# Kernel optimization log

Hardware: AMD Instinct MI355X
Metric: run time of the kernel (lower is better)

## Reference

```python
import jax, jax.numpy as jnp
import numpy as np

# Jamba mamba mixer dims
H = 4096      # hidden_size
D = 8192      # intermediate_size = mamba_expand * hidden_size
N = 16        # ssm_state_size (mamba_d_state)
K = 4         # conv_kernel_size (mamba_d_conv)
R = 256       # time_step_rank (mamba_dt_rank)
BATCH = 1
L = 2048
EPS = 1e-6


def setup_inputs() -> dict:
    key = jax.random.key(0)
    ks = jax.random.split(key, 10)
    s = 0.02
    return {
        "hidden_states": jax.random.normal(ks[0], (BATCH, L, H), jnp.float32),
        "W_in": jax.random.normal(ks[1], (2 * D, H), jnp.float32) * s,
        "conv_w": jax.random.normal(ks[2], (D, K), jnp.float32) * s,
        "conv_b": jax.random.normal(ks[3], (D,), jnp.float32) * s,
        "Wx": jax.random.normal(ks[4], (R + 2 * N, D), jnp.float32) * s,
        "dt_ln_w": jnp.ones((R,), jnp.float32),
        "b_ln_w": jnp.ones((N,), jnp.float32),
        "c_ln_w": jnp.ones((N,), jnp.float32),
        "Wdt": jax.random.normal(ks[5], (D, R), jnp.float32) * s,
        "dt_bias": jax.random.normal(ks[6], (D,), jnp.float32) * s,
        "A": -jnp.exp(jax.random.normal(ks[7], (D, N), jnp.float32) * 0.5),  # A = -exp(A_log)
        "D_param": jnp.ones((D,), jnp.float32),
        "W_out": jax.random.normal(ks[8], (H, D), jnp.float32) * s,
    }


def _rmsnorm(x, w):
    return x * jax.lax.rsqrt(jnp.mean(x * x, axis=-1, keepdims=True) + EPS) * w


def reference(hidden_states, W_in, conv_w, conv_b, Wx, dt_ln_w, b_ln_w, c_ln_w,
              Wdt, dt_bias, A, D_param, W_out):
    # in_proj -> [B, L, 2D]; split into ssm branch and gate
    proj = hidden_states @ W_in.T
    u, gate = jnp.split(proj, 2, axis=-1)

    # causal depthwise conv1d over sequence dim, then SiLU (causal_conv1d_fn)
    x = jnp.transpose(u, (0, 2, 1))  # [B, D, L]
    x = jax.lax.conv_general_dilated(
        x, conv_w[:, None, :], window_strides=(1,), padding=[(K - 1, 0)],
        dimension_numbers=("NCH", "OIH", "NCH"), feature_group_count=D)
    u = jax.nn.silu(jnp.transpose(x, (0, 2, 1)) + conv_b)  # [B, L, D]

    # x_proj -> dt / B / C with RMSNorms
    ssm_p = u @ Wx.T  # [B, L, R + 2N]
    dt, Bm, Cm = jnp.split(ssm_p, [R, R + N], axis=-1)
    dt = _rmsnorm(dt, dt_ln_w)
    Bm = _rmsnorm(Bm, b_ln_w)
    Cm = _rmsnorm(Cm, c_ln_w)

    # dt_proj (skip_bias_add: bias folded into softplus, delta_softplus=True)
    delta = jax.nn.softplus(dt @ Wdt.T + dt_bias)  # [B, L, D]

    # selective scan: state [B, D, N], recurrence over L
    def step(state, xs):
        d_t, B_t, C_t, u_t = xs  # [B,D], [B,N], [B,N], [B,D]
        dA = jnp.exp(d_t[..., None] * A)                       # [B, D, N]
        state = dA * state + (d_t * u_t)[..., None] * B_t[:, None, :]
        y_t = jnp.einsum("bdn,bn->bd", state, C_t)
        return state, y_t

    init = jnp.zeros((hidden_states.shape[0], D, N), hidden_states.dtype)
    xs = (jnp.swapaxes(delta, 0, 1), jnp.swapaxes(Bm, 0, 1),
          jnp.swapaxes(Cm, 0, 1), jnp.swapaxes(u, 0, 1))
    _, ys = jax.lax.scan(step, init, xs)  # ys: [L, B, D]

    y = jnp.swapaxes(ys, 0, 1) + u * D_param   # skip connection u * D
    y = y * jax.nn.silu(gate)                  # gated output
    return y @ W_out.T                         # out_proj -> [B, L, H]
```

## Files before the change

### kernel.cpp

```cpp
#include <hip/hip_runtime.h>
#include <stdint.h>


#define LSEQ 2048
#define HDIM 4096
#define DDIM 8192
#define NST  16
#define NPAD 384
#define NC   16
#define CLEN 128

typedef __bf16 bf16x8 __attribute__((ext_vector_type(8)));
typedef float  f32x4  __attribute__((ext_vector_type(4)));

__device__ __forceinline__ ushort f2b(float f) {
  uint32_t x = __float_as_uint(f);
  x += 0x7FFFu + ((x >> 16) & 1u);
  return (ushort)(x >> 16);
}
__device__ __forceinline__ float b2f(ushort u) {
  return __uint_as_float(((uint32_t)u) << 16);
}

__device__ __forceinline__ void gload_lds16(const ushort* g, ushort* l) {
  __builtin_amdgcn_global_load_lds(
      (const __attribute__((address_space(1))) void*)g,
      (__attribute__((address_space(3))) void*)l, 16, 0, 0);
}

__global__ __launch_bounds__(256) void cvt_kernel(const float* __restrict__ s,
                                                  ushort* __restrict__ d,
                                                  size_t n8) {
  size_t i = (size_t)blockIdx.x * 256 + threadIdx.x;
  if (i >= n8) return;
  const float4* sp = (const float4*)s;
  float4 a = sp[2 * i], b = sp[2 * i + 1];
  union { ushort us[8]; uint4 v; } u;
  u.us[0] = f2b(a.x); u.us[1] = f2b(a.y); u.us[2] = f2b(a.z); u.us[3] = f2b(a.w);
  u.us[4] = f2b(b.x); u.us[5] = f2b(b.y); u.us[6] = f2b(b.z); u.us[7] = f2b(b.w);
  ((uint4*)d)[i] = u.v;
}

template <int MODE, int OUT>
__global__ __launch_bounds__(512, 2) void gemm8p(
    const ushort* __restrict__ A, const ushort* __restrict__ Bw,
    void* __restrict__ Cv, int M, int N, int ldk, int Kc) {
  __shared__ __align__(16) ushort As[2][256 * 64];
  __shared__ __align__(16) ushort Bs[2][256 * 64];
  const int tid  = threadIdx.x;
  const int lane = tid & 63;
  const int w    = tid >> 6;
  const int wr   = w >> 2;
  const int wc   = w & 3;

  const int glob = (blockIdx.z * gridDim.y + blockIdx.y) * gridDim.x + blockIdx.x;
  const int k8 = glob & 7, j = glob >> 3;
  int mt, nt, zz;
  if (MODE == 0) {
    mt = j & 7;
    nt = k8 * (gridDim.x >> 3) + (j >> 3);
    zz = 0;
  } else {
    mt = j & 7;
    nt = (k8 >> 1) * 4 + (j >> 3);
    zz = k8 & 1;
  }
  const int m0 = mt * 256, n0 = nt * 256;
  const int kbeg = zz * Kc;
  const int NT = Kc >> 6;

  const int srck = (lane & 7) ^ ((lane >> 3) & 7);
  const int astripe = w >> 2, awl = w & 3;
  const int arow_st = astripe * 128 + awl * 8 + (lane >> 3);
  const ushort* Abase = A + (size_t)(m0 + arow_st) * ldk + kbeg + srck * 8;
  const int aldsb = (astripe * 128 + awl * 8) * 64;
  const int brow_st = w * 8 + (lane >> 3);
  const ushort* Bbase = Bw + (size_t)(n0 + brow_st) * ldk + kbeg + srck * 8;
  const int bldsb = (w * 8) * 64;

  const int lrow = lane & 15;
  const int kch  = lane >> 4;
  const int axor = lrow & 7;

  auto stA = [&](int buf, int kt, int q) {
    gload_lds16(Abase + (size_t)q * 32 * ldk + kt * 64,
                &As[buf][aldsb + q * 32 * 64]);
  };
  auto stB = [&](int buf, int kt, int half, int jj) {
    gload_lds16(Bbase + (size_t)(half * 128 + jj * 64) * ldk + kt * 64,
                &Bs[buf][bldsb + (half * 128 + jj * 64) * 64]);
  };
  auto rdA = [&](int buf, int mi, int sl) -> bf16x8 {
    int arow = wr * 128 + mi * 16 + lrow;
    int s4 = sl * 4 + kch;
    return *(const bf16x8*)&As[buf][arow * 64 + ((s4 ^ axor) << 3)];
  };
  auto rdB = [&](int buf, int ni, int sl) -> bf16x8 {
    int brow = wc * 64 + ni * 16 + lrow;
    int s4 = sl * 4 + kch;
    return *(const bf16x8*)&Bs[buf][brow * 64 + ((s4 ^ axor) << 3)];
  };

  f32x4 acc[8][4] = {};
  bf16x8 afr[2][2][2];
  bf16x8 bfr[2][4][2];

#define RDAQ(BUF, Q, AP)                                                      \
  { _Pragma("unroll") for (int m2 = 0; m2 < 2; ++m2)                          \
      _Pragma("unroll") for (int sl = 0; sl < 2; ++sl)                        \
        afr[AP][m2][sl] = rdA(BUF, (Q) * 2 + m2, sl); }
#define RDBALL(BUF, BP)                                                       \
  { _Pragma("unroll") for (int ni = 0; ni < 4; ++ni)                          \
      _Pragma("unroll") for (int sl = 0; sl < 2; ++sl)                        \
        bfr[BP][ni][sl] = rdB(BUF, ni, sl); }
#define MFMA16(MQ, AP, BP)                                                    \
  { asm volatile("s_barrier" ::: "memory");                                   \
    __builtin_amdgcn_s_setprio(1);                                            \
    _Pragma("unroll") for (int sl = 0; sl < 2; ++sl)                          \
      _Pragma("unroll") for (int m2 = 0; m2 < 2; ++m2)                        \
        _Pragma("unroll") for (int ni = 0; ni < 4; ++ni)                      \
          acc[(MQ) * 2 + m2][ni] = __builtin_amdgcn_mfma_f32_16x16x32_bf16(   \
              afr[AP][m2][sl], bfr[BP][ni][sl], acc[(MQ) * 2 + m2][ni],       \
              0, 0, 0);                                                       \
    __builtin_amdgcn_s_setprio(0); }

  stB(0, 0, 0, 0); stB(0, 0, 0, 1); stB(0, 0, 1, 0); stB(0, 0, 1, 1);
  stA(0, 0, 0); stA(0, 0, 1); stA(0, 0, 2); stA(0, 0, 3);
  stB(1, 1, 0, 0); stB(1, 1, 0, 1); stB(1, 1, 1, 0); stB(1, 1, 1, 1);
  stA(1, 1, 0); stA(1, 1, 1); stA(1, 1, 2); stA(1, 1, 3);
  asm volatile("s_waitcnt vmcnt(8)" ::: "memory");
  asm volatile("s_barrier" ::: "memory");
  RDBALL(0, 0);
  RDAQ(0, 0, 1);

  for (int t = 0; t < NT; t += 2) {
    const int t2 = (t + 2 < NT) ? t + 2 : 0;
    const int t3 = (t + 3 < NT) ? t + 3 : 0;
    RDAQ(0, 1, 0);
    stB(0, t2, 0, 0); stB(0, t2, 0, 1);
    MFMA16(0, 1, 0);
    RDAQ(0, 2, 1);
    stB(0, t2, 1, 0); stB(0, t2, 1, 1);
    MFMA16(1, 0, 0);
    RDAQ(0, 3, 0);
    stA(0, t2, 0); stA(0, t2, 1);
    MFMA16(2, 1, 0);
    asm volatile("s_waitcnt vmcnt(6)" ::: "memory");
    RDBALL(1, 1);
    RDAQ(1, 0, 1);
    stA(0, t2, 2); stA(0, t2, 3);
    MFMA16(3, 0, 0);
    RDAQ(1, 1, 0);
    stB(1, t3, 0, 0); stB(1, t3, 0, 1);
    MFMA16(0, 1, 1);
    RDAQ(1, 2, 1);
    stB(1, t3, 1, 0); stB(1, t3, 1, 1);
    MFMA16(1, 0, 1);
    RDAQ(1, 3, 0);
    stA(1, t3, 0); stA(1, t3, 1);
    MFMA16(2, 1, 1);
    asm volatile("s_waitcnt vmcnt(6)" ::: "memory");
    RDBALL(0, 0);
    RDAQ(0, 0, 1);
    stA(1, t3, 2); stA(1, t3, 3);
    MFMA16(3, 0, 1);
  }
#undef RDAQ
#undef RDBALL
#undef MFMA16

  asm volatile("s_waitcnt vmcnt(0)" ::: "memory");
  float*  C  = (float*) Cv + (size_t)zz * M * N;
  ushort* Cb = (ushort*)Cv + (size_t)zz * M * N;
#pragma unroll
  for (int mi = 0; mi < 8; ++mi) {
    int row0 = m0 + wr * 128 + mi * 16 + kch * 4;
#pragma unroll
    for (int ni = 0; ni < 4; ++ni) {
      int col = n0 + wc * 64 + ni * 16 + lrow;
#pragma unroll
      for (int q_ = 0; q_ < 4; ++q_) {
        if (OUT == 0)
          C[(size_t)(row0 + q_) * N + col] = acc[mi][ni][q_];
        else
          Cb[(size_t)(row0 + q_) * N + col] = f2b(acc[mi][ni][q_]);
      }
    }
  }
}

template <int EPI, int OBF>
__global__ __launch_bounds__(256) void gemm_nt(
    const ushort* __restrict__ A, const ushort* __restrict__ Bw,
    void* __restrict__ Cv, int M, int N, int ldk, int Kc,
    const float* __restrict__ bias) {
  __shared__ __align__(16) ushort As[128 * 64];
  __shared__ __align__(16) ushort Bs[128 * 64];
  const int tid  = threadIdx.x;
  const int lane = tid & 63;
  const int wid  = tid >> 6;
  const int wr = wid >> 1, wc = wid & 1;
  const int m0 = blockIdx.y * 128, n0 = blockIdx.x * 128;
  const int kbeg = blockIdx.z * Kc;
  float*  C  = (float*) Cv + (size_t)blockIdx.z * M * N;
  ushort* Cb = (ushort*)Cv + (size_t)blockIdx.z * M * N;
  const int rr0 = tid >> 3;
  const int sl  = tid & 7;
  const int lrow = lane & 15;
  const int lks  = lane >> 4;

  f32x4 acc[4][4] = {};

  for (int k0 = kbeg; k0 < kbeg + Kc; k0 += 64) {
#pragma unroll
    for (int i = 0; i < 4; ++i) {
      int rr  = i * 32 + rr0;
      int ksl = sl ^ (rr & 7);
      const ushort* ga = A  + (size_t)(m0 + rr) * ldk + k0 + ksl * 8;
      const ushort* gb = Bw + (size_t)(n0 + rr) * ldk + k0 + ksl * 8;
      ushort* la = As + (i * 256 + (wid << 6)) * 8;
      ushort* lb = Bs + (i * 256 + (wid << 6)) * 8;
      gload_lds16(ga, la);
      gload_lds16(gb, lb);
    }
    __syncthreads();
#pragma unroll
    for (int kc = 0; kc < 2; ++kc) {
      bf16x8 av[4], bv[4];
#pragma unroll
      for (int mi = 0; mi < 4; ++mi) {
        int row = wr * 64 + mi * 16 + lrow;
        int ks  = kc * 4 + lks;
        av[mi] = *(const bf16x8*)(As + row * 64 + ((ks ^ (row & 7)) << 3));
      }
#pragma unroll
      for (int ni = 0; ni < 4; ++ni) {
        int row = wc * 64 + ni * 16 + lrow;
        int ks  = kc * 4 + lks;
        bv[ni] = *(const bf16x8*)(Bs + row * 64 + ((ks ^ (row & 7)) << 3));
      }
#pragma unroll
      for (int mi = 0; mi < 4; ++mi)
#pragma unroll
        for (int ni = 0; ni < 4; ++ni)
          acc[mi][ni] = __builtin_amdgcn_mfma_f32_16x16x32_bf16(
              av[mi], bv[ni], acc[mi][ni], 0, 0, 0);
    }
    __syncthreads();
  }

#pragma unroll
  for (int mi = 0; mi < 4; ++mi) {
    int row0 = m0 + wr * 64 + mi * 16 + (lks << 2);
#pragma unroll
    for (int ni = 0; ni < 4; ++ni) {
      int col = n0 + wc * 64 + ni * 16 + lrow;
      float bcol = 0.f;
      if (EPI == 1) bcol = bias[col];
#pragma unroll
      for (int q = 0; q < 4; ++q) {
        float v = acc[mi][ni][q];
        if (EPI == 1) {
          v += bcol;
          v = (v > 20.f) ? v : log1pf(__expf(v));
        }
        if (OBF == 0) C [(size_t)(row0 + q) * N + col] = v;
        else          Cb[(size_t)(row0 + q) * N + col] = f2b(v);
      }
    }
  }
}

__global__ __launch_bounds__(256) void reduce2_kernel(
    const float* __restrict__ Cp, float* __restrict__ out) {
  size_t i = (size_t)blockIdx.x * 256 + threadIdx.x;
  const size_t MN4 = (size_t)LSEQ * HDIM / 4;
  float4 a = ((const float4*)Cp)[i];
  float4 b = ((const float4*)Cp)[MN4 + i];
  ((float4*)out)[i] = make_float4(a.x + b.x, a.y + b.y, a.z + b.z, a.w + b.w);
}

__global__ __launch_bounds__(256) void conv_silu_kernel(
    const ushort* __restrict__ ub, const float* __restrict__ cw,
    const float* __restrict__ cb, ushort* __restrict__ uc) {
  int d = blockIdx.x * 256 + threadIdx.x;
  int l0 = blockIdx.y * 16;
  float4 w4 = ((const float4*)cw)[d];
  float bsum = cb[d];
  float xm3 = (l0 >= 3) ? b2f(ub[(size_t)(l0 - 3) * DDIM + d]) : 0.f;
  float xm2 = (l0 >= 2) ? b2f(ub[(size_t)(l0 - 2) * DDIM + d]) : 0.f;
  float xm1 = (l0 >= 1) ? b2f(ub[(size_t)(l0 - 1) * DDIM + d]) : 0.f;
#pragma unroll
  for (int i = 0; i < 16; ++i) {
    int l = l0 + i;
    float xc = b2f(ub[(size_t)l * DDIM + d]);
    float s = bsum + w4.x * xm3 + w4.y * xm2 + w4.z * xm1 + w4.w * xc;
    float o = s / (1.f + __expf(-s));
    uc[(size_t)l * DDIM + d] = f2b(o);
    xm3 = xm2; xm2 = xm1; xm1 = xc;
  }
}

__global__ __launch_bounds__(64) void norms_kernel(
    const float* __restrict__ Cp, const float* __restrict__ dtw,
    const float* __restrict__ bw, const float* __restrict__ cwn,
    ushort* __restrict__ dtn, float* __restrict__ Bn, float* __restrict__ Cn) {
  int l = blockIdx.x, lane = threadIdx.x;
  const size_t MN = (size_t)LSEQ * NPAD;
  const float* row = Cp + (size_t)l * NPAD;
  float va[4] = {0.f, 0.f, 0.f, 0.f};
#pragma unroll
  for (int z = 0; z < 8; ++z) {
    float4 v = ((const float4*)(row + z * MN))[lane];
    va[0] += v.x; va[1] += v.y; va[2] += v.z; va[3] += v.w;
  }
  float ss = va[0]*va[0] + va[1]*va[1] + va[2]*va[2] + va[3]*va[3];
#pragma unroll
  for (int m = 32; m >= 1; m >>= 1) ss += __shfl_xor(ss, m);
  float rs = rsqrtf(ss * (1.f / 256.f) + 1e-6f);
  float4 wv = ((const float4*)dtw)[lane];
  float wa[4] = {wv.x, wv.y, wv.z, wv.w};
  union { ushort us[4]; uint2 v2; } o;
#pragma unroll
  for (int jj = 0; jj < 4; ++jj) o.us[jj] = f2b(va[jj] * rs * wa[jj]);
  ((uint2*)(dtn + (size_t)l * 256))[lane] = o.v2;

  int g = lane & 15;
  float bv = 0.f, cv = 0.f;
#pragma unroll
  for (int z = 0; z < 8; ++z) {
    bv += row[z * MN + 256 + g];
    cv += row[z * MN + 272 + g];
  }
  float bs = bv * bv, cs = cv * cv;
#pragma unroll
  for (int m = 8; m >= 1; m >>= 1) {
    bs += __shfl_xor(bs, m);
    cs += __shfl_xor(cs, m);
  }
  if (lane < 16) {
    Bn[(size_t)l * NST + lane] = bv * rsqrtf(bs * (1.f / 16.f) + 1e-6f) * bw[lane];
    Cn[(size_t)l * NST + lane] = cv * rsqrtf(cs * (1.f / 16.f) + 1e-6f) * cwn[lane];
  }
}

__global__ __launch_bounds__(256) void scan_phase1(
    const ushort* __restrict__ delta, const ushort* __restrict__ uc,
    const float* __restrict__ Bn, const float* __restrict__ Am,
    float* __restrict__ Sbuf, float* __restrict__ Pbuf) {
  __shared__ float sB[CLEN * NST];
  const int tid = threadIdx.x;
  const int d = blockIdx.x * 256 + tid;
  const int c = blockIdx.y, l0 = c * CLEN;
  {
    const float4* bsrc = (const float4*)(Bn + (size_t)l0 * NST);
    float4* bdst = (float4*)sB;
    for (int i = tid; i < CLEN * NST / 4; i += 256) bdst[i] = bsrc[i];
  }
  __syncthreads();
  float A[16];
#pragma unroll
  for (int jj = 0; jj < 4; ++jj) {
    float4 a4 = ((const float4*)(Am + (size_t)d * NST))[jj];
    A[4*jj] = a4.x; A[4*jj+1] = a4.y; A[4*jj+2] = a4.z; A[4*jj+3] = a4.w;
  }
  float st[16] = {};
  float sd = 0.f;
  const size_t base = (size_t)l0 * DDIM + d;
  float dx0 = b2f(delta[base]),  dx1 = b2f(delta[base + DDIM]);
  float ux0 = b2f(uc[base]),     ux1 = b2f(uc[base + DDIM]);
  for (int l = 0; l < CLEN; l += 2) {
    int lp = (l + 2 < CLEN) ? l + 2 : CLEN - 2;
    float dxn0 = b2f(delta[base + (size_t)lp * DDIM]);
    float dxn1 = b2f(delta[base + (size_t)(lp + 1) * DDIM]);
    float uxn0 = b2f(uc[base + (size_t)lp * DDIM]);
    float uxn1 = b2f(uc[base + (size_t)(lp + 1) * DDIM]);
    sd += dx0;
    float dxu = dx0 * ux0;
#pragma unroll
    for (int n = 0; n < 16; ++n)
      st[n] = fmaf(__expf(dx0 * A[n]), st[n], dxu * sB[l * NST + n]);
    sd += dx1;
    dxu = dx1 * ux1;
#pragma unroll
    for (int n = 0; n < 16; ++n)
      st[n] = fmaf(__expf(dx1 * A[n]), st[n], dxu * sB[(l + 1) * NST + n]);
    dx0 = dxn0; dx1 = dxn1; ux0 = uxn0; ux1 = uxn1;
  }
  float4* Sd = (float4*)(Sbuf + ((size_t)c * DDIM + d) * NST);
  float4* Pd = (float4*)(Pbuf + ((size_t)c * DDIM + d) * NST);
#pragma unroll
  for (int jj = 0; jj < 4; ++jj) {
    Sd[jj] = make_float4(st[4*jj], st[4*jj+1], st[4*jj+2], st[4*jj+3]);
    Pd[jj] = make_float4(__expf(A[4*jj] * sd),   __expf(A[4*jj+1] * sd),
                         __expf(A[4*jj+2] * sd), __expf(A[4*jj+3] * sd));
  }
}

__global__ __launch_bounds__(256) void scan_phase2(
    const float* __restrict__ Sbuf, float* __restrict__ Pbuf) {
  size_t t = (size_t)blockIdx.x * 256 + threadIdx.x;
  const size_t stride = (size_t)DDIM * NST;
  float s = 0.f;
  for (int c = 0; c < NC; ++c) {
    float P = Pbuf[c * stride + t];
    float S = Sbuf[c * stride + t];
    Pbuf[c * stride + t] = s;
    s = fmaf(P, s, S);
  }
}

__global__ __launch_bounds__(256) void scan_phase3(
    const ushort* __restrict__ delta, const ushort* __restrict__ uc,
    const float* __restrict__ Bn, const float* __restrict__ Cn,
    const float* __restrict__ Am, const float* __restrict__ Ibuf,
    const ushort* __restrict__ gb, const float* __restrict__ Dp,
    ushort* __restrict__ yg) {
  __shared__ float sB[CLEN * NST];
  __shared__ float sC[CLEN * NST];
  const int tid = threadIdx.x;
  const int d = blockIdx.x * 256 + tid;
  const int c = blockIdx.y, l0 = c * CLEN;
  {
    const float4* bsrc = (const float4*)(Bn + (size_t)l0 * NST);
    const float4* csrc = (const float4*)(Cn + (size_t)l0 * NST);
    float4* bdst = (float4*)sB;
    float4* cdst = (float4*)sC;
    for (int i = tid; i < CLEN * NST / 4; i += 256) {
      bdst[i] = bsrc[i];
      cdst[i] = csrc[i];
    }
  }
  __syncthreads();
  float A[16], st[16];
#pragma unroll
  for (int jj = 0; jj < 4; ++jj) {
    float4 a4 = ((const float4*)(Am + (size_t)d * NST))[jj];
    A[4*jj] = a4.x; A[4*jj+1] = a4.y; A[4*jj+2] = a4.z; A[4*jj+3] = a4.w;
    float4 s4 = ((const float4*)(Ibuf + ((size_t)c * DDIM + d) * NST))[jj];
    st[4*jj] = s4.x; st[4*jj+1] = s4.y; st[4*jj+2] = s4.z; st[4*jj+3] = s4.w;
  }
  const float Dpd = Dp[d];
  const size_t base = (size_t)l0 * DDIM + d;
  float dx0 = b2f(delta[base]),   dx1 = b2f(delta[base + DDIM]);
  float ux0 = b2f(uc[base]),      ux1 = b2f(uc[base + DDIM]);
  float g0  = b2f(gb[base]),      g1  = b2f(gb[base + DDIM]);
  for (int l = 0; l < CLEN; l += 2) {
    int lp = (l + 2 < CLEN) ? l + 2 : CLEN - 2;
    float dxn0 = b2f(delta[base + (size_t)lp * DDIM]);
    float dxn1 = b2f(delta[base + (size_t)(lp + 1) * DDIM]);
    float uxn0 = b2f(uc[base + (size_t)lp * DDIM]);
    float uxn1 = b2f(uc[base + (size_t)(lp + 1) * DDIM]);
    float gn0  = b2f(gb[base + (size_t)lp * DDIM]);
    float gn1  = b2f(gb[base + (size_t)(lp + 1) * DDIM]);
    {
      float dxu = dx0 * ux0, y0 = 0.f, y1 = 0.f;
#pragma unroll
      for (int n = 0; n < 16; n += 2) {
        st[n]   = fmaf(__expf(dx0 * A[n]),   st[n],   dxu * sB[l * NST + n]);
        st[n+1] = fmaf(__expf(dx0 * A[n+1]), st[n+1], dxu * sB[l * NST + n+1]);
        y0 = fmaf(st[n],   sC[l * NST + n],   y0);
        y1 = fmaf(st[n+1], sC[l * NST + n+1], y1);
      }
      float o = (y0 + y1 + ux0 * Dpd) * (g0 / (1.f + __expf(-g0)));
      yg[base + (size_t)l * DDIM] = f2b(o);
    }
    {
      float dxu = dx1 * ux1, y0 = 0.f, y1 = 0.f;
#pragma unroll
      for (int n = 0; n < 16; n += 2) {
        st[n]   = fmaf(__expf(dx1 * A[n]),   st[n],   dxu * sB[(l+1) * NST + n]);
        st[n+1] = fmaf(__expf(dx1 * A[n+1]), st[n+1], dxu * sB[(l+1) * NST + n+1]);
        y0 = fmaf(st[n],   sC[(l+1) * NST + n],   y0);
        y1 = fmaf(st[n+1], sC[(l+1) * NST + n+1], y1);
      }
      float o = (y0 + y1 + ux1 * Dpd) * (g1 / (1.f + __expf(-g1)));
      yg[base + (size_t)(l + 1) * DDIM] = f2b(o);
    }
    dx0 = dxn0; dx1 = dxn1; ux0 = uxn0; ux1 = uxn1; g0 = gn0; g1 = gn1;
  }
}

extern "C" void kernel_launch(void* const* d_in, const int* in_sizes, int n_in,
                              void* d_out, int out_size, void* d_ws, size_t ws_size,
                              hipStream_t stream) {
  (void)in_sizes; (void)n_in; (void)out_size; (void)ws_size;
  const float* hs   = (const float*)d_in[0];
  const float* W_in = (const float*)d_in[1];
  const float* cw   = (const float*)d_in[2];
  const float* cb   = (const float*)d_in[3];
  const float* Wx   = (const float*)d_in[4];
  const float* dtw  = (const float*)d_in[5];
  const float* bw   = (const float*)d_in[6];
  const float* cwn  = (const float*)d_in[7];
  const float* Wdt  = (const float*)d_in[8];
  const float* dtb  = (const float*)d_in[9];
  const float* Am   = (const float*)d_in[10];
  const float* Dp   = (const float*)d_in[11];
  const float* Wout = (const float*)d_in[12];
  float* out = (float*)d_out;

  char* ws = (char*)d_ws;
  const size_t MB = 1ull << 20;
  ushort* win_b   = (ushort*)(ws);
  ushort* delta_b = (ushort*)(ws);
  ushort* wout_b  = (ushort*)(ws + 64 * MB);
  ushort* ubuf   = (ushort*)(ws + 128 * MB);
  float*  Cp     = (float*) (ws + 128 * MB);
  float*  Cp2    = (float*) (ws + 128 * MB);
  float*  Sbuf   = (float*) (ws + 152 * MB);
  float*  Pbuf   = (float*) (ws + 160 * MB);
  ushort* gbuf   = (ushort*)(ws + 192 * MB);
  ushort* hs_b   = (ushort*)(ws + 256 * MB);
  ushort* wxp_b  = (ushort*)(ws + 272 * MB);
  ushort* wdt_b  = (ushort*)(ws + 278 * MB);
  ushort* ucv    = (ushort*)(ws + 282 * MB);
  ushort* dtn    = (ushort*)(ws + 317 * MB);
  float*  Bn     = (float*) (ws + 318 * MB);
  float*  Cn     = (float*) (ws + 318 * MB + 131072);
  ushort* yg     = (ushort*)(ws + 319 * MB);

  cvt_kernel<<<67108864 / 2048, 256, 0, stream>>>(W_in, win_b, 67108864 / 8);
  cvt_kernel<<<8388608 / 2048, 256, 0, stream>>>(hs, hs_b, 8388608 / 8);
  cvt_kernel<<<2359296 / 2048, 256, 0, stream>>>(Wx, wxp_b, 2359296 / 8);
  hipMemsetAsync((char*)wxp_b + 4718592, 0, 1572864, stream);
  cvt_kernel<<<2097152 / 2048, 256, 0, stream>>>(Wdt, wdt_b, 2097152 / 8);

  gemm8p<0, 1><<<dim3(32, 8), 512, 0, stream>>>(hs_b, win_b, ubuf,
                                                2048, DDIM, 4096, 4096);
  gemm8p<0, 1><<<dim3(32, 8), 512, 0, stream>>>(hs_b, win_b + (size_t)DDIM * 4096,
                                                gbuf, 2048, DDIM, 4096, 4096);
  cvt_kernel<<<33554432 / 2048, 256, 0, stream>>>(Wout, wout_b, 33554432 / 8);

  conv_silu_kernel<<<dim3(32, 128), 256, 0, stream>>>(ubuf, cw, cb, ucv);

  gemm_nt<0, 0><<<dim3(3, 16, 8), 256, 0, stream>>>(ucv, wxp_b, Cp,
                                                    2048, NPAD, 8192, 1024,
                                                    nullptr);
  norms_kernel<<<2048, 64, 0, stream>>>(Cp, dtw, bw, cwn, dtn, Bn, Cn);

  gemm_nt<1, 1><<<dim3(64, 16), 256, 0, stream>>>(dtn, wdt_b, delta_b,
                                                  2048, DDIM, 256, 256, dtb);

  scan_phase1<<<dim3(32, NC), 256, 0, stream>>>(delta_b, ucv, Bn, Am, Sbuf, Pbuf);
  scan_phase2<<<512, 256, 0, stream>>>(Sbuf, Pbuf);
  scan_phase3<<<dim3(32, NC), 256, 0, stream>>>(delta_b, ucv, Bn, Cn, Am, Pbuf,
                                                gbuf, Dp, yg);

  gemm8p<1, 0><<<dim3(16, 8, 2), 512, 0, stream>>>(yg, wout_b, Cp2,
                                                   2048, HDIM, 8192, 4096);
  reduce2_kernel<<<(LSEQ * HDIM / 4) / 256, 256, 0, stream>>>(Cp2, out);
}
```

Before: 824.3 us.

## Merge in_proj GEMMs, widen x_proj split-K, vectorize scan over channel pairs

The two in_proj GEMM launches become one launch that uses blockIdx.z to pick the weight half and output buffer. The x_proj split-K factor goes from 8 to 16, and the norms reduction is updated to match. The scan kernels now handle two channels per thread with packed 32-bit bf16 loads and stores, and the chunk count doubles to 32 chunks of 64 steps, which moves the Sbuf/Pbuf workspace. Each thread carries 32 state registers, which can lower occupancy, and the larger split-K adds partial-sum traffic.

```diff
diff --git a/kernel.cpp b/kernel.cpp
--- a/kernel.cpp
+++ b/kernel.cpp
@@ -7,8 +7,9 @@
 #define DDIM 8192
 #define NST  16
 #define NPAD 384
-#define NC   16
-#define CLEN 128
+#define NC   32
+#define CLEN 64
+#define XZK  16
 
 typedef __bf16 bf16x8 __attribute__((ext_vector_type(8)));
 typedef float  f32x4  __attribute__((ext_vector_type(4)));
@@ -20,6 +21,12 @@
 }
 __device__ __forceinline__ float b2f(ushort u) {
   return __uint_as_float(((uint32_t)u) << 16);
+}
+__device__ __forceinline__ float b2f_lo(uint u) {
+  return __uint_as_float(u << 16);
+}
+__device__ __forceinline__ float b2f_hi(uint u) {
+  return __uint_as_float(u & 0xFFFF0000u);
 }
 
 __device__ __forceinline__ void gload_lds16(const ushort* g, ushort* l) {
@@ -44,7 +51,8 @@
 template <int MODE, int OUT>
 __global__ __launch_bounds__(512, 2) void gemm8p(
     const ushort* __restrict__ A, const ushort* __restrict__ Bw,
-    void* __restrict__ Cv, int M, int N, int ldk, int Kc) {
+    void* __restrict__ Cv, int M, int N, int ldk, int Kc,
+    size_t bOffZ, size_t cOffZ) {
   __shared__ __align__(16) ushort As[2][256 * 64];
   __shared__ __align__(16) ushort Bs[2][256 * 64];
   const int tid  = threadIdx.x;
@@ -53,14 +61,19 @@
   const int wr   = w >> 2;
   const int wc   = w & 3;
 
-  const int glob = (blockIdx.z * gridDim.y + blockIdx.y) * gridDim.x + blockIdx.x;
-  const int k8 = glob & 7, j = glob >> 3;
   int mt, nt, zz;
+  size_t boff = 0, coff = 0;
   if (MODE == 0) {
+    const int bid2 = blockIdx.y * gridDim.x + blockIdx.x;
+    const int k8 = bid2 & 7, j = bid2 >> 3;
     mt = j & 7;
     nt = k8 * (gridDim.x >> 3) + (j >> 3);
     zz = 0;
+    boff = (size_t)blockIdx.z * bOffZ;
+    coff = (size_t)blockIdx.z * cOffZ;
   } else {
+    const int glob = (blockIdx.z * gridDim.y + blockIdx.y) * gridDim.x + blockIdx.x;
+    const int k8 = glob & 7, j = glob >> 3;
     mt = j & 7;
     nt = (k8 >> 1) * 4 + (j >> 3);
     zz = k8 & 1;
@@ -75,7 +88,7 @@
   const ushort* Abase = A + (size_t)(m0 + arow_st) * ldk + kbeg + srck * 8;
   const int aldsb = (astripe * 128 + awl * 8) * 64;
   const int brow_st = w * 8 + (lane >> 3);
-  const ushort* Bbase = Bw + (size_t)(n0 + brow_st) * ldk + kbeg + srck * 8;
+  const ushort* Bbase = Bw + boff + (size_t)(n0 + brow_st) * ldk + kbeg + srck * 8;
   const int bldsb = (w * 8) * 64;
 
   const int lrow = lane & 15;
@@ -170,8 +183,8 @@
 #undef MFMA16
 
   asm volatile("s_waitcnt vmcnt(0)" ::: "memory");
-  float*  C  = (float*) Cv + (size_t)zz * M * N;
-  ushort* Cb = (ushort*)Cv + (size_t)zz * M * N;
+  float*  C  = (float*) Cv + (size_t)zz * M * N + coff;
+  ushort* Cb = (ushort*)Cv + (size_t)zz * M * N + coff;
 #pragma unroll
   for (int mi = 0; mi < 8; ++mi) {
     int row0 = m0 + wr * 128 + mi * 16 + kch * 4;
@@ -310,7 +323,7 @@
   const float* row = Cp + (size_t)l * NPAD;
   float va[4] = {0.f, 0.f, 0.f, 0.f};
 #pragma unroll
-  for (int z = 0; z < 8; ++z) {
+  for (int z = 0; z < XZK; ++z) {
     float4 v = ((const float4*)(row + z * MN))[lane];
     va[0] += v.x; va[1] += v.y; va[2] += v.z; va[3] += v.w;
   }
@@ -328,7 +341,7 @@
   int g = lane & 15;
   float bv = 0.f, cv = 0.f;
 #pragma unroll
-  for (int z = 0; z < 8; ++z) {
+  for (int z = 0; z < XZK; ++z) {
     bv += row[z * MN + 256 + g];
     cv += row[z * MN + 272 + g];
   }
@@ -350,7 +363,7 @@
     float* __restrict__ Sbuf, float* __restrict__ Pbuf) {
   __shared__ float sB[CLEN * NST];
   const int tid = threadIdx.x;
-  const int d = blockIdx.x * 256 + tid;
+  const int d0 = (blockIdx.x * 256 + tid) * 2;
   const int c = blockIdx.y, l0 = c * CLEN;
   {
     const float4* bsrc = (const float4*)(Bn + (size_t)l0 * NST);
@@ -358,39 +371,57 @@
     for (int i = tid; i < CLEN * NST / 4; i += 256) bdst[i] = bsrc[i];
   }
   __syncthreads();
-  float A[16];
-#pragma unroll
-  for (int jj = 0; jj < 4; ++jj) {
-    float4 a4 = ((const float4*)(Am + (size_t)d * NST))[jj];
+  float A[32];
+#pragma unroll
+  for (int jj = 0; jj < 8; ++jj) {
+    float4 a4 = ((const float4*)(Am + (size_t)d0 * NST))[jj];
     A[4*jj] = a4.x; A[4*jj+1] = a4.y; A[4*jj+2] = a4.z; A[4*jj+3] = a4.w;
   }
-  float st[16] = {};
-  float sd = 0.f;
-  const size_t base = (size_t)l0 * DDIM + d;
-  float dx0 = b2f(delta[base]),  dx1 = b2f(delta[base + DDIM]);
-  float ux0 = b2f(uc[base]),     ux1 = b2f(uc[base + DDIM]);
+  float st[32] = {};
+  float sda = 0.f, sdb = 0.f;
+  const size_t base = ((size_t)l0 * DDIM + d0) >> 1;
+  const uint* d32 = (const uint*)delta;
+  const uint* u32 = (const uint*)uc;
+  const size_t LD2 = DDIM / 2;
+  uint dx0 = d32[base], dx1 = d32[base + LD2];
+  uint ux0 = u32[base], ux1 = u32[base + LD2];
   for (int l = 0; l < CLEN; l += 2) {
     int lp = (l + 2 < CLEN) ? l + 2 : CLEN - 2;
-    float dxn0 = b2f(delta[base + (size_t)lp * DDIM]);
-    float dxn1 = b2f(delta[base + (size_t)(lp + 1) * DDIM]);
-    float uxn0 = b2f(uc[base + (size_t)lp * DDIM]);
-    float uxn1 = b2f(uc[base + (size_t)(lp + 1) * DDIM]);
-    sd += dx0;
-    float dxu = dx0 * ux0;
-#pragma unroll
-    for (int n = 0; n < 16; ++n)
-      st[n] = fmaf(__expf(dx0 * A[n]), st[n], dxu * sB[l * NST + n]);
-    sd += dx1;
-    dxu = dx1 * ux1;
-#pragma unroll
-    for (int n = 0; n < 16; ++n)
-      st[n] = fmaf(__expf(dx1 * A[n]), st[n], dxu * sB[(l + 1) * NST + n]);
+    uint dxn0 = d32[base + (size_t)lp * LD2];
+    uint dxn1 = d32[base + (size_t)(lp + 1) * LD2];
+    uint uxn0 = u32[base + (size_t)lp * LD2];
+    uint uxn1 = u32[base + (size_t)(lp + 1) * LD2];
+    {
+      float da = b2f_lo(dx0), db = b2f_hi(dx0);
+      float ua = b2f_lo(ux0), ub = b2f_hi(ux0);
+      sda += da; sdb += db;
+      float dua = da * ua, dub = db * ub;
+#pragma unroll
+      for (int n = 0; n < 16; ++n) {
+        float bn = sB[l * NST + n];
+        st[n]      = fmaf(__expf(da * A[n]),      st[n],      dua * bn);
+        st[16 + n] = fmaf(__expf(db * A[16 + n]), st[16 + n], dub * bn);
+      }
+    }
+    {
+      float da = b2f_lo(dx1), db = b2f_hi(dx1);
+      float ua = b2f_lo(ux1), ub = b2f_hi(ux1);
+      sda += da; sdb += db;
+      float dua = da * ua, dub = db * ub;
+#pragma unroll
+      for (int n = 0; n < 16; ++n) {
+        float bn = sB[(l + 1) * NST + n];
+        st[n]      = fmaf(__expf(da * A[n]),      st[n],      dua * bn);
+        st[16 + n] = fmaf(__expf(db * A[16 + n]), st[16 + n], dub * bn);
+      }
+    }
     dx0 = dxn0; dx1 = dxn1; ux0 = uxn0; ux1 = uxn1;
   }
-  float4* Sd = (float4*)(Sbuf + ((size_t)c * DDIM + d) * NST);
-  float4* Pd = (float4*)(Pbuf + ((size_t)c * DDIM + d) * NST);
-#pragma unroll
-  for (int jj = 0; jj < 4; ++jj) {
+  float4* Sd = (float4*)(Sbuf + ((size_t)c * DDIM + d0) * NST);
+  float4* Pd = (float4*)(Pbuf + ((size_t)c * DDIM + d0) * NST);
+#pragma unroll
+  for (int jj = 0; jj < 8; ++jj) {
+    float sd = (jj < 4) ? sda : sdb;
     Sd[jj] = make_float4(st[4*jj], st[4*jj+1], st[4*jj+2], st[4*jj+3]);
     Pd[jj] = make_float4(__expf(A[4*jj] * sd),   __expf(A[4*jj+1] * sd),
                          __expf(A[4*jj+2] * sd), __expf(A[4*jj+3] * sd));
@@ -419,7 +450,7 @@
   __shared__ float sB[CLEN * NST];
   __shared__ float sC[CLEN * NST];
   const int tid = threadIdx.x;
-  const int d = blockIdx.x * 256 + tid;
+  const int d0 = (blockIdx.x * 256 + tid) * 2;
   const int c = blockIdx.y, l0 = c * CLEN;
   {
     const float4* bsrc = (const float4*)(Bn + (size_t)l0 * NST);
@@ -432,50 +463,67 @@
     }
   }
   __syncthreads();
-  float A[16], st[16];
-#pragma unroll
-  for (int jj = 0; jj < 4; ++jj) {
-    float4 a4 = ((const float4*)(Am + (size_t)d * NST))[jj];
+  float A[32], st[32];
+#pragma unroll
+  for (int jj = 0; jj < 8; ++jj) {
+    float4 a4 = ((const float4*)(Am + (size_t)d0 * NST))[jj];
     A[4*jj] = a4.x; A[4*jj+1] = a4.y; A[4*jj+2] = a4.z; A[4*jj+3] = a4.w;
-    float4 s4 = ((const float4*)(Ibuf + ((size_t)c * DDIM + d) * NST))[jj];
+    float4 s4 = ((const float4*)(Ibuf + ((size_t)c * DDIM + d0) * NST))[jj];
     st[4*jj] = s4.x; st[4*jj+1] = s4.y; st[4*jj+2] = s4.z; st[4*jj+3] = s4.w;
   }
-  const float Dpd = Dp[d];
-  const size_t base = (size_t)l0 * DDIM + d;
-  float dx0 = b2f(delta[base]),   dx1 = b2f(delta[base + DDIM]);
-  float ux0 = b2f(uc[base]),      ux1 = b2f(uc[base + DDIM]);
-  float g0  = b2f(gb[base]),      g1  = b2f(gb[base + DDIM]);
+  const float2 Dp2 = ((const float2*)Dp)[d0 >> 1];
+  const size_t base = ((size_t)l0 * DDIM + d0) >> 1;
+  const uint* d32 = (const uint*)delta;
+  const uint* u32 = (const uint*)uc;
+  const uint* g32 = (const uint*)gb;
+  uint* y32 = (uint*)yg;
+  const size_t LD2 = DDIM / 2;
+  uint dx0 = d32[base], dx1 = d32[base + LD2];
+  uint ux0 = u32[base], ux1 = u32[base + LD2];
+  uint g0  = g32[base], g1  = g32[base + LD2];
   for (int l = 0; l < CLEN; l += 2) {
     int lp = (l + 2 < CLEN) ? l + 2 : CLEN - 2;
-    float dxn0 = b2f(delta[base + (size_t)lp * DDIM]);
-    float dxn1 = b2f(delta[base + (size_t)(lp + 1) * DDIM]);
-    float uxn0 = b2f(uc[base + (size_t)lp * DDIM]);
-    float uxn1 = b2f(uc[base + (size_t)(lp + 1) * DDIM]);
-    float gn0  = b2f(gb[base + (size_t)lp * DDIM]);
-    float gn1  = b2f(gb[base + (size_t)(lp + 1) * DDIM]);
+    uint dxn0 = d32[base + (size_t)lp * LD2];
+    uint dxn1 = d32[base + (size_t)(lp + 1) * LD2];
+    uint uxn0 = u32[base + (size_t)lp * LD2];
+    uint uxn1 = u32[base + (size_t)(lp + 1) * LD2];
+    uint gn0  = g32[base + (size_t)lp * LD2];
+    uint gn1  = g32[base + (size_t)(lp + 1) * LD2];
     {
-      float dxu = dx0 * ux0, y0 = 0.f, y1 = 0.f;
-#pragma unroll
-      for (int n = 0; n < 16; n += 2) {
-        st[n]   = fmaf(__expf(dx0 * A[n]),   st[n],   dxu * sB[l * NST + n]);
-        st[n+1] = fmaf(__expf(dx0 * A[n+1]), st[n+1], dxu * sB[l * NST + n+1]);
-        y0 = fmaf(st[n],   sC[l * NST + n],   y0);
-        y1 = fmaf(st[n+1], sC[l * NST + n+1], y1);
-      }
-      float o = (y0 + y1 + ux0 * Dpd) * (g0 / (1.f + __expf(-g0)));
-      yg[base + (size_t)l * DDIM] = f2b(o);
+      float da = b2f_lo(dx0), db = b2f_hi(dx0);
+      float ua = b2f_lo(ux0), ub = b2f_hi(ux0);
+      float ga = b2f_lo(g0),  gbv = b2f_hi(g0);
+      float dua = da * ua, dub = db * ub;
+      float ya = 0.f, yb = 0.f;
+#pragma unroll
+      for (int n = 0; n < 16; ++n) {
+        float bn = sB[l * NST + n], cn = sC[l * NST + n];
+        st[n]      = fmaf(__expf(da * A[n]),      st[n],      dua * bn);
+        st[16 + n] = fmaf(__expf(db * A[16 + n]), st[16 + n], dub * bn);
+        ya = fmaf(st[n], cn, ya);
+        yb = fmaf(st[16 + n], cn, yb);
+      }
+      float oa = (ya + ua * Dp2.x) * (ga / (1.f + __expf(-ga)));
+      float ob = (yb + ub * Dp2.y) * (gbv / (1.f + __expf(-gbv)));
+      y32[base + (size_t)l * LD2] = (uint)f2b(oa) | ((uint)f2b(ob) << 16);
     }
     {
-      float dxu = dx1 * ux1, y0 = 0.f, y1 = 0.f;
-#pragma unroll
-      for (int n = 0; n < 16; n += 2) {
-        st[n]   = fmaf(__expf(dx1 * A[n]),   st[n],   dxu * sB[(l+1) * NST + n]);
-        st[n+1] = fmaf(__expf(dx1 * A[n+1]), st[n+1], dxu * sB[(l+1) * NST + n+1]);
-        y0 = fmaf(st[n],   sC[(l+1) * NST + n],   y0);
-        y1 = fmaf(st[n+1], sC[(l+1) * NST + n+1], y1);
-      }
-      float o = (y0 + y1 + ux1 * Dpd) * (g1 / (1.f + __expf(-g1)));
-      yg[base + (size_t)(l + 1) * DDIM] = f2b(o);
+      float da = b2f_lo(dx1), db = b2f_hi(dx1);
+      float ua = b2f_lo(ux1), ub = b2f_hi(ux1);
+      float ga = b2f_lo(g1),  gbv = b2f_hi(g1);
+      float dua = da * ua, dub = db * ub;
+      float ya = 0.f, yb = 0.f;
+#pragma unroll
+      for (int n = 0; n < 16; ++n) {
+        float bn = sB[(l + 1) * NST + n], cn = sC[(l + 1) * NST + n];
+        st[n]      = fmaf(__expf(da * A[n]),      st[n],      dua * bn);
+        st[16 + n] = fmaf(__expf(db * A[16 + n]), st[16 + n], dub * bn);
+        ya = fmaf(st[n], cn, ya);
+        yb = fmaf(st[16 + n], cn, yb);
+      }
+      float oa = (ya + ua * Dp2.x) * (ga / (1.f + __expf(-ga)));
+      float ob = (yb + ub * Dp2.y) * (gbv / (1.f + __expf(-gbv)));
+      y32[base + (size_t)(l + 1) * LD2] = (uint)f2b(oa) | ((uint)f2b(ob) << 16);
     }
     dx0 = dxn0; dx1 = dxn1; ux0 = uxn0; ux1 = uxn1; g0 = gn0; g1 = gn1;
   }
@@ -508,9 +556,9 @@
   ushort* ubuf   = (ushort*)(ws + 128 * MB);
   float*  Cp     = (float*) (ws + 128 * MB);
   float*  Cp2    = (float*) (ws + 128 * MB);
-  float*  Sbuf   = (float*) (ws + 152 * MB);
-  float*  Pbuf   = (float*) (ws + 160 * MB);
+  float*  Sbuf   = (float*) (ws + 176 * MB);
   ushort* gbuf   = (ushort*)(ws + 192 * MB);
+  float*  Pbuf   = (float*) (ws + 224 * MB);
   ushort* hs_b   = (ushort*)(ws + 256 * MB);
   ushort* wxp_b  = (ushort*)(ws + 272 * MB);
   ushort* wdt_b  = (ushort*)(ws + 278 * MB);
@@ -526,28 +574,27 @@
   hipMemsetAsync((char*)wxp_b + 4718592, 0, 1572864, stream);
   cvt_kernel<<<2097152 / 2048, 256, 0, stream>>>(Wdt, wdt_b, 2097152 / 8);
 
-  gemm8p<0, 1><<<dim3(32, 8), 512, 0, stream>>>(hs_b, win_b, ubuf,
-                                                2048, DDIM, 4096, 4096);
-  gemm8p<0, 1><<<dim3(32, 8), 512, 0, stream>>>(hs_b, win_b + (size_t)DDIM * 4096,
-                                                gbuf, 2048, DDIM, 4096, 4096);
+  gemm8p<0, 1><<<dim3(32, 8, 2), 512, 0, stream>>>(
+      hs_b, win_b, ubuf, 2048, DDIM, 4096, 4096,
+      (size_t)DDIM * 4096, (size_t)(gbuf - ubuf));
   cvt_kernel<<<33554432 / 2048, 256, 0, stream>>>(Wout, wout_b, 33554432 / 8);
 
   conv_silu_kernel<<<dim3(32, 128), 256, 0, stream>>>(ubuf, cw, cb, ucv);
 
-  gemm_nt<0, 0><<<dim3(3, 16, 8), 256, 0, stream>>>(ucv, wxp_b, Cp,
-                                                    2048, NPAD, 8192, 1024,
-                                                    nullptr);
+  gemm_nt<0, 0><<<dim3(3, 16, XZK), 256, 0, stream>>>(ucv, wxp_b, Cp,
+                                                      2048, NPAD, 8192,
+                                                      8192 / XZK, nullptr);
   norms_kernel<<<2048, 64, 0, stream>>>(Cp, dtw, bw, cwn, dtn, Bn, Cn);
 
   gemm_nt<1, 1><<<dim3(64, 16), 256, 0, stream>>>(dtn, wdt_b, delta_b,
                                                   2048, DDIM, 256, 256, dtb);
 
-  scan_phase1<<<dim3(32, NC), 256, 0, stream>>>(delta_b, ucv, Bn, Am, Sbuf, Pbuf);
+  scan_phase1<<<dim3(16, NC), 256, 0, stream>>>(delta_b, ucv, Bn, Am, Sbuf, Pbuf);
   scan_phase2<<<512, 256, 0, stream>>>(Sbuf, Pbuf);
-  scan_phase3<<<dim3(32, NC), 256, 0, stream>>>(delta_b, ucv, Bn, Cn, Am, Pbuf,
+  scan_phase3<<<dim3(16, NC), 256, 0, stream>>>(delta_b, ucv, Bn, Cn, Am, Pbuf,
                                                 gbuf, Dp, yg);
 
   gemm8p<1, 0><<<dim3(16, 8, 2), 512, 0, stream>>>(yg, wout_b, Cp2,
-                                                   2048, HDIM, 8192, 4096);
+                                                   2048, HDIM, 8192, 4096, 0, 0);
   reduce2_kernel<<<(LSEQ * HDIM / 4) / 256, 256, 0, stream>>>(Cp2, out);
 }
```

Result: no change. 825.7 us (+0.2%).
